# Optimization experiments

Measured on AMD Instinct MI355X. Metric: run time of the kernel, lower is better.

The kernel has to match this reference:

```python
import jax, jax.numpy as jnp
import numpy as np

L, B, D = 8192, 4096, 1024


def setup_inputs() -> dict:
    key = jax.random.key(0)
    k1, k2, k3, k4 = jax.random.split(key, 4)
    return {
        "q_hat": jax.random.normal(k1, (L, D), dtype=jnp.float32),
        "q_real": jax.random.normal(k2, (L, D), dtype=jnp.float32),
        "encoded_gt": jax.random.normal(k3, (B, D), dtype=jnp.float32),
        "encoded_pred": jax.random.normal(k4, (B, D), dtype=jnp.float32),
    }


def reference(q_hat, q_real, encoded_gt, encoded_pred):
    # local_loss: -(1/L) * sum_i dot(q_hat[i], q_real[i])
    # (replaces the Python loop of L tiny torch.dot launches with one fused reduce)
    local = -jnp.mean(jnp.sum(q_hat * q_real, axis=-1))

    # global_loss: sum_{i,j} max(0, <pred_i, gt_j> - <pred_i, gt_i> + 1)
    # (replaces the O(B^2) double loop of torch.dot calls with one GEMM)
    scores = jnp.einsum("id,jd->ij", encoded_pred, encoded_gt)  # [B, B]
    pos = jnp.diagonal(scores)                                   # [B]
    margin = jnp.float32(1.0)
    glob = jnp.sum(jnp.maximum(0.0, scores - pos[:, None] + margin))

    return local + glob
```

## Files before the change

kernel.cpp:

```cpp
#include <hip/hip_runtime.h>
#include <hip/hip_bf16.h>

#define LROWS 8192
#define BROWS 4096
#define DDIM  1024

typedef __attribute__((ext_vector_type(4)))  int   i32x4;
typedef __attribute__((ext_vector_type(8)))  int   i32x8;
typedef __attribute__((ext_vector_type(16))) float f32x16;

typedef const unsigned int __attribute__((address_space(1))) gu32;
typedef unsigned int       __attribute__((address_space(3))) su32;

__device__ inline unsigned int pack_fp8x4(float4 v) {
    unsigned int w = 0;
    w = __builtin_amdgcn_cvt_pk_fp8_f32(v.x, v.y, w, false);
    w = __builtin_amdgcn_cvt_pk_fp8_f32(v.z, v.w, w, true);
    return w;
}

__global__ __launch_bounds__(256) void prep_kernel(
    const float4* __restrict__ pred,
    const float4* __restrict__ gt,
    unsigned int* __restrict__ opred,
    unsigned int* __restrict__ ogt,
    float* __restrict__ pos,
    float* __restrict__ out) {
    __shared__ float sred[4];
    const int row = blockIdx.x;
    const int t = threadIdx.x;
    if (row == 0 && t == 0) out[0] = 0.0f;

    const int idx = row * 256 + t;
    float4 p = pred[idx];
    float4 g = gt[idx];
    opred[idx] = pack_fp8x4(p);
    ogt[idx]   = pack_fp8x4(g);
    float s = p.x * g.x + p.y * g.y + p.z * g.z + p.w * g.w;

    #pragma unroll
    for (int o = 32; o > 0; o >>= 1) s += __shfl_down(s, o, 64);
    if ((t & 63) == 0) sred[t >> 6] = s;
    __syncthreads();
    if (t == 0) pos[row] = sred[0] + sred[1] + sred[2] + sred[3];
}

__global__ __launch_bounds__(512, 2) void hinge_gemm(
    const unsigned char* __restrict__ A,
    const unsigned char* __restrict__ Bm,
    const float* __restrict__ pos,
    const float4* __restrict__ qh,
    const float4* __restrict__ qr,
    float* __restrict__ out) {
    extern __shared__ unsigned char smem[];
    unsigned char* const As = smem;
    unsigned char* const Bs = smem + 65536;
    float* const pos_s = (float*)(smem + 131072);
    float* const sred  = (float*)(smem + 132096);
    float* const sred2 = (float*)(smem + 132128);

    const int orig = blockIdx.x;
    const int xk = orig & 7, xj = orig >> 3;
    const int bm = (xk >> 1) * 4 + (xj >> 3);
    const int bn = (xk & 1) * 8 + (xj & 7);

    const int tid = threadIdx.x;
    const int lane = tid & 63;
    const int wave = tid >> 6;
    const int wm = wave >> 2;
    const int wn = wave & 3;

    const int grow = lane >> 3;
    const int usw  = (lane & 7) ^ grow;

    const unsigned char* Abase = A  + (size_t)(bm * 256) * DDIM;
    const unsigned char* Bbase = Bm + (size_t)(bn * 256) * DDIM;

    const float4* qhb = qh + (size_t)orig * 8192;
    const float4* qrb = qr + (size_t)orig * 8192;

    f32x16 acc[4][2];
    #pragma unroll
    for (int i = 0; i < 4; i++)
        #pragma unroll
        for (int j = 0; j < 2; j++)
            #pragma unroll
            for (int r = 0; r < 16; r++) acc[i][j][r] = 0.0f;

    const int sc1 = 0x7f7f7f7f;
    const int mrow = lane & 31;
    const int kh = lane >> 5;

    auto stage_one = [&](int buf, int k0, int i) {
        const int c = wave * 4 + i;
        const int row = c * 8 + grow;
        __builtin_amdgcn_global_load_lds(
            (gu32*)(Abase + (size_t)row * DDIM + k0 + usw * 16),
            (su32*)(As + buf * 32768 + c * 1024), 16, 0, 0);
        __builtin_amdgcn_global_load_lds(
            (gu32*)(Bbase + (size_t)row * DDIM + k0 + usw * 16),
            (su32*)(Bs + buf * 32768 + c * 1024), 16, 0, 0);
    };

    auto compute = [&](int buf) {
        const unsigned char* Ab = As + buf * 32768;
        const unsigned char* Bb = Bs + buf * 32768;
        #pragma unroll
        for (int h = 0; h < 2; h++) {
            const int u0 = h * 4 + kh * 2;
            i32x8 af[4];
            i32x8 bg[2];
            #pragma unroll
            for (int mt = 0; mt < 4; mt++) {
                const int r = wm * 128 + mt * 32 + mrow;
                i32x4 x0 = *(const i32x4*)&Ab[r * 128 + ((u0    ) ^ (r & 7)) * 16];
                i32x4 x1 = *(const i32x4*)&Ab[r * 128 + ((u0 + 1) ^ (r & 7)) * 16];
                af[mt] = __builtin_shufflevector(x0, x1, 0, 1, 2, 3, 4, 5, 6, 7);
            }
            #pragma unroll
            for (int nt = 0; nt < 2; nt++) {
                const int r = wn * 64 + nt * 32 + mrow;
                i32x4 x0 = *(const i32x4*)&Bb[r * 128 + ((u0    ) ^ (r & 7)) * 16];
                i32x4 x1 = *(const i32x4*)&Bb[r * 128 + ((u0 + 1) ^ (r & 7)) * 16];
                bg[nt] = __builtin_shufflevector(x0, x1, 0, 1, 2, 3, 4, 5, 6, 7);
            }
            __builtin_amdgcn_s_setprio(1);
            #pragma unroll
            for (int mt = 0; mt < 4; mt++)
                #pragma unroll
                for (int nt = 0; nt < 2; nt++)
                    acc[mt][nt] = __builtin_amdgcn_mfma_scale_f32_32x32x64_f8f6f4(
                        af[mt], bg[nt], acc[mt][nt], 0, 0, 0, sc1, 0, sc1);
            __builtin_amdgcn_s_setprio(0);
        }
    };

    float ls = 0.0f;
    float4 ch0, ch1, cr0, cr1;
    float4 nh0, nh1, nr0, nr1;

    if (tid < 256) pos_s[tid] = pos[bm * 256 + tid];
    #pragma unroll
    for (int i = 0; i < 4; i++) stage_one(0, 0, i);
    __builtin_amdgcn_sched_barrier(0);
    ch0 = qhb[tid];       ch1 = qhb[tid + 512];
    cr0 = qrb[tid];       cr1 = qrb[tid + 512];
    asm volatile("s_waitcnt vmcnt(4) lgkmcnt(0)" ::: "memory");
    __builtin_amdgcn_s_barrier();

    int p = 0;
    for (int t = 0; t < 7; ++t) {
        const int k0n = (t + 1) * 128;
        const unsigned char* Ab = As + p * 32768;
        const unsigned char* Bb = Bs + p * 32768;
        #pragma unroll
        for (int h = 0; h < 2; ++h) {
            const int u0 = h * 4 + kh * 2;
            i32x8 af0, af1, af2, af3, bg0, bg1;
            {
                const int r = wm * 128 + 0 * 32 + mrow;
                i32x4 x0 = *(const i32x4*)&Ab[r * 128 + ((u0    ) ^ (r & 7)) * 16];
                i32x4 x1 = *(const i32x4*)&Ab[r * 128 + ((u0 + 1) ^ (r & 7)) * 16];
                af0 = __builtin_shufflevector(x0, x1, 0, 1, 2, 3, 4, 5, 6, 7);
            }
            {
                const int r = wm * 128 + 1 * 32 + mrow;
                i32x4 x0 = *(const i32x4*)&Ab[r * 128 + ((u0    ) ^ (r & 7)) * 16];
                i32x4 x1 = *(const i32x4*)&Ab[r * 128 + ((u0 + 1) ^ (r & 7)) * 16];
                af1 = __builtin_shufflevector(x0, x1, 0, 1, 2, 3, 4, 5, 6, 7);
            }
            {
                const int r = wm * 128 + 2 * 32 + mrow;
                i32x4 x0 = *(const i32x4*)&Ab[r * 128 + ((u0    ) ^ (r & 7)) * 16];
                i32x4 x1 = *(const i32x4*)&Ab[r * 128 + ((u0 + 1) ^ (r & 7)) * 16];
                af2 = __builtin_shufflevector(x0, x1, 0, 1, 2, 3, 4, 5, 6, 7);
            }
            {
                const int r = wm * 128 + 3 * 32 + mrow;
                i32x4 x0 = *(const i32x4*)&Ab[r * 128 + ((u0    ) ^ (r & 7)) * 16];
                i32x4 x1 = *(const i32x4*)&Ab[r * 128 + ((u0 + 1) ^ (r & 7)) * 16];
                af3 = __builtin_shufflevector(x0, x1, 0, 1, 2, 3, 4, 5, 6, 7);
            }
            {
                const int r = wn * 64 + 0 * 32 + mrow;
                i32x4 x0 = *(const i32x4*)&Bb[r * 128 + ((u0    ) ^ (r & 7)) * 16];
                i32x4 x1 = *(const i32x4*)&Bb[r * 128 + ((u0 + 1) ^ (r & 7)) * 16];
                bg0 = __builtin_shufflevector(x0, x1, 0, 1, 2, 3, 4, 5, 6, 7);
            }
            {
                const int r = wn * 64 + 1 * 32 + mrow;
                i32x4 x0 = *(const i32x4*)&Bb[r * 128 + ((u0    ) ^ (r & 7)) * 16];
                i32x4 x1 = *(const i32x4*)&Bb[r * 128 + ((u0 + 1) ^ (r & 7)) * 16];
                bg1 = __builtin_shufflevector(x0, x1, 0, 1, 2, 3, 4, 5, 6, 7);
            }
            stage_one(p ^ 1, k0n, h * 2);
            stage_one(p ^ 1, k0n, h * 2 + 1);
            if (h == 1) {
                __builtin_amdgcn_sched_barrier(0);
                const int qo = (t + 1) * 1024 + tid;
                nh0 = qhb[qo];       nh1 = qhb[qo + 512];
                nr0 = qrb[qo];       nr1 = qrb[qo + 512];
                ls += ch0.x * cr0.x + ch0.y * cr0.y + ch0.z * cr0.z + ch0.w * cr0.w
                    + ch1.x * cr1.x + ch1.y * cr1.y + ch1.z * cr1.z + ch1.w * cr1.w;
            }
            __builtin_amdgcn_s_barrier();
            __builtin_amdgcn_s_setprio(1);
            acc[0][0] = __builtin_amdgcn_mfma_scale_f32_32x32x64_f8f6f4(af0, bg0, acc[0][0], 0, 0, 0, sc1, 0, sc1);
            acc[0][1] = __builtin_amdgcn_mfma_scale_f32_32x32x64_f8f6f4(af0, bg1, acc[0][1], 0, 0, 0, sc1, 0, sc1);
            acc[1][0] = __builtin_amdgcn_mfma_scale_f32_32x32x64_f8f6f4(af1, bg0, acc[1][0], 0, 0, 0, sc1, 0, sc1);
            acc[1][1] = __builtin_amdgcn_mfma_scale_f32_32x32x64_f8f6f4(af1, bg1, acc[1][1], 0, 0, 0, sc1, 0, sc1);
            acc[2][0] = __builtin_amdgcn_mfma_scale_f32_32x32x64_f8f6f4(af2, bg0, acc[2][0], 0, 0, 0, sc1, 0, sc1);
            acc[2][1] = __builtin_amdgcn_mfma_scale_f32_32x32x64_f8f6f4(af2, bg1, acc[2][1], 0, 0, 0, sc1, 0, sc1);
            acc[3][0] = __builtin_amdgcn_mfma_scale_f32_32x32x64_f8f6f4(af3, bg0, acc[3][0], 0, 0, 0, sc1, 0, sc1);
            acc[3][1] = __builtin_amdgcn_mfma_scale_f32_32x32x64_f8f6f4(af3, bg1, acc[3][1], 0, 0, 0, sc1, 0, sc1);
            __builtin_amdgcn_s_setprio(0);
            if (h == 1) {
                asm volatile("s_waitcnt vmcnt(4)" ::: "memory");
            }
            __builtin_amdgcn_s_barrier();
        }
        ch0 = nh0; ch1 = nh1; cr0 = nr0; cr1 = nr1;
        p ^= 1;
    }
    ls += ch0.x * cr0.x + ch0.y * cr0.y + ch0.z * cr0.z + ch0.w * cr0.w
        + ch1.x * cr1.x + ch1.y * cr1.y + ch1.z * cr1.z + ch1.w * cr1.w;
    compute(p);

    float s = 0.0f;
    const int rq = 4 * kh;
    #pragma unroll
    for (int mt = 0; mt < 4; mt++) {
        #pragma unroll
        for (int nt = 0; nt < 2; nt++) {
            #pragma unroll
            for (int i = 0; i < 16; i++) {
                const int lr = wm * 128 + mt * 32 + (i & 3) + 8 * (i >> 2) + rq;
                const float v = acc[mt][nt][i] - pos_s[lr] + 1.0f;
                s += fmaxf(v, 0.0f);
            }
        }
    }
    #pragma unroll
    for (int o = 32; o > 0; o >>= 1) {
        s  += __shfl_down(s, o, 64);
        ls += __shfl_down(ls, o, 64);
    }
    if (lane == 0) { sred[wave] = s; sred2[wave] = ls; }
    __syncthreads();
    if (tid == 0) {
        float tot = 0.0f, lp = 0.0f;
        #pragma unroll
        for (int w = 0; w < 8; w++) { tot += sred[w]; lp += sred2[w]; }
        atomicAdd(out, tot - lp * (1.0f / (float)LROWS));
    }
}

extern "C" void kernel_launch(void* const* d_in, const int* in_sizes, int n_in,
                              void* d_out, int out_size, void* d_ws, size_t ws_size,
                              hipStream_t stream) {
    const float* q_hat  = (const float*)d_in[0];
    const float* q_real = (const float*)d_in[1];
    const float* gt     = (const float*)d_in[2];
    const float* pred   = (const float*)d_in[3];
    float* out = (float*)d_out;

    char* ws = (char*)d_ws;
    unsigned char* pred_8 = (unsigned char*)ws;
    unsigned char* gt_8   = (unsigned char*)(ws + (size_t)BROWS * DDIM);
    float* pos   = (float*)(ws + (size_t)2 * BROWS * DDIM);

    hipLaunchKernelGGL(prep_kernel, dim3(BROWS), dim3(256), 0, stream,
                       (const float4*)pred, (const float4*)gt,
                       (unsigned int*)pred_8, (unsigned int*)gt_8,
                       pos, out);

    const size_t lds_bytes = 131072 + 1024 + 64;
    hipLaunchKernelGGL(hinge_gemm, dim3(256), dim3(512), lds_bytes, stream,
                       pred_8, gt_8, pos,
                       (const float4*)q_hat, (const float4*)q_real, out);
}
```

Baseline: 131.2 us.

## Fuse fp8 prep and hinge GEMM into one cooperative kernel with grid sync

```diff
diff --git a/kernel.cpp b/kernel.cpp
--- a/kernel.cpp
+++ b/kernel.cpp
@@ -1,5 +1,8 @@
 #include <hip/hip_runtime.h>
 #include <hip/hip_bf16.h>
+#include <hip/hip_cooperative_groups.h>
+
+namespace cg = cooperative_groups;
 
 #define LROWS 8192
 #define BROWS 4096
@@ -19,36 +22,12 @@
     return w;
 }
 
-__global__ __launch_bounds__(256) void prep_kernel(
+__global__ __launch_bounds__(512, 2) void fused_kernel(
     const float4* __restrict__ pred,
     const float4* __restrict__ gt,
     unsigned int* __restrict__ opred,
     unsigned int* __restrict__ ogt,
     float* __restrict__ pos,
-    float* __restrict__ out) {
-    __shared__ float sred[4];
-    const int row = blockIdx.x;
-    const int t = threadIdx.x;
-    if (row == 0 && t == 0) out[0] = 0.0f;
-
-    const int idx = row * 256 + t;
-    float4 p = pred[idx];
-    float4 g = gt[idx];
-    opred[idx] = pack_fp8x4(p);
-    ogt[idx]   = pack_fp8x4(g);
-    float s = p.x * g.x + p.y * g.y + p.z * g.z + p.w * g.w;
-
-    #pragma unroll
-    for (int o = 32; o > 0; o >>= 1) s += __shfl_down(s, o, 64);
-    if ((t & 63) == 0) sred[t >> 6] = s;
-    __syncthreads();
-    if (t == 0) pos[row] = sred[0] + sred[1] + sred[2] + sred[3];
-}
-
-__global__ __launch_bounds__(512, 2) void hinge_gemm(
-    const unsigned char* __restrict__ A,
-    const unsigned char* __restrict__ Bm,
-    const float* __restrict__ pos,
     const float4* __restrict__ qh,
     const float4* __restrict__ qr,
     float* __restrict__ out) {
@@ -59,12 +38,37 @@
     float* const sred  = (float*)(smem + 132096);
     float* const sred2 = (float*)(smem + 132128);
 
+    const int tid = threadIdx.x;
+
+    {
+        if (blockIdx.x == 0 && tid == 0) out[0] = 0.0f;
+        const int rowg = blockIdx.x * 16 + (tid >> 5);
+        const int col  = tid & 31;
+        float s = 0.0f;
+        #pragma unroll
+        for (int j = 0; j < 8; ++j) {
+            const int idx = rowg * 256 + col + j * 32;
+            float4 p = pred[idx];
+            float4 g = gt[idx];
+            opred[idx] = pack_fp8x4(p);
+            ogt[idx]   = pack_fp8x4(g);
+            s += p.x * g.x + p.y * g.y + p.z * g.z + p.w * g.w;
+        }
+        #pragma unroll
+        for (int o = 16; o > 0; o >>= 1) s += __shfl_down(s, o, 32);
+        if (col == 0) pos[rowg] = s;
+    }
+    __threadfence();
+    cg::this_grid().sync();
+
+    const unsigned char* const A  = (const unsigned char*)opred;
+    const unsigned char* const Bm = (const unsigned char*)ogt;
+
     const int orig = blockIdx.x;
     const int xk = orig & 7, xj = orig >> 3;
     const int bm = (xk >> 1) * 4 + (xj >> 3);
     const int bn = (xk & 1) * 8 + (xj & 7);
 
-    const int tid = threadIdx.x;
     const int lane = tid & 63;
     const int wave = tid >> 6;
     const int wm = wave >> 2;
@@ -258,24 +262,25 @@
 extern "C" void kernel_launch(void* const* d_in, const int* in_sizes, int n_in,
                               void* d_out, int out_size, void* d_ws, size_t ws_size,
                               hipStream_t stream) {
-    const float* q_hat  = (const float*)d_in[0];
-    const float* q_real = (const float*)d_in[1];
-    const float* gt     = (const float*)d_in[2];
-    const float* pred   = (const float*)d_in[3];
+    const float4* q_hat  = (const float4*)d_in[0];
+    const float4* q_real = (const float4*)d_in[1];
+    const float4* gt     = (const float4*)d_in[2];
+    const float4* pred   = (const float4*)d_in[3];
     float* out = (float*)d_out;
 
     char* ws = (char*)d_ws;
-    unsigned char* pred_8 = (unsigned char*)ws;
-    unsigned char* gt_8   = (unsigned char*)(ws + (size_t)BROWS * DDIM);
+    unsigned int* pred_8 = (unsigned int*)ws;
+    unsigned int* gt_8   = (unsigned int*)(ws + (size_t)BROWS * DDIM);
     float* pos   = (float*)(ws + (size_t)2 * BROWS * DDIM);
 
-    hipLaunchKernelGGL(prep_kernel, dim3(BROWS), dim3(256), 0, stream,
-                       (const float4*)pred, (const float4*)gt,
-                       (unsigned int*)pred_8, (unsigned int*)gt_8,
-                       pos, out);
-
-    const size_t lds_bytes = 131072 + 1024 + 64;
-    hipLaunchKernelGGL(hinge_gemm, dim3(256), dim3(512), lds_bytes, stream,
-                       pred_8, gt_8, pos,
-                       (const float4*)q_hat, (const float4*)q_real, out);
+    const unsigned int lds_bytes = 131072 + 1024 + 64;
+    void* args[] = {
+        (void*)&pred, (void*)&gt,
+        (void*)&pred_8, (void*)&gt_8,
+        (void*)&pos,
+        (void*)&q_hat, (void*)&q_real,
+        (void*)&out,
+    };
+    hipLaunchCooperativeKernel((const void*)fused_kernel, dim3(256), dim3(512),
+                               args, lds_bytes, stream);
 }
```

Measured after the change: 225.7 us. 1.72x slower.
